# Performance work log

Measured on AMD Instinct MI355X. Metric: run time of the kernel, lower is better.

Reference implementation:

```python
import jax, jax.numpy as jnp
import numpy as np

B, T, IN, H = 128, 1024, 256, 512


def setup_inputs() -> dict:
    key = jax.random.key(0)
    ks = jax.random.split(key, 16)
    w = lambda k, shape: (jax.random.normal(k, shape, jnp.float32) * 0.02)
    inp = {"embed": jax.random.normal(ks[0], (B, T, IN), jnp.float32)}
    in_dims = [IN, H, H]
    for l in range(3):
        inp[f"w_ih{l+1}"] = w(ks[1 + 4 * l], (4 * H, in_dims[l]))
        inp[f"w_hh{l+1}"] = w(ks[2 + 4 * l], (4 * H, H))
        inp[f"b_ih{l+1}"] = w(ks[3 + 4 * l], (4 * H,))
        inp[f"b_hh{l+1}"] = w(ks[4 + 4 * l], (4 * H,))
    inp["fc_w"] = w(ks[13], (IN, H))
    inp["fc_b"] = w(ks[14], (IN,))
    return inp


def _lstm_cell(x, h, c, w_ih, w_hh, b):
    # PyTorch LSTMCell: gates ordered (i, f, g, o)
    gates = x @ w_ih.T + h @ w_hh.T + b  # [B, 4H]
    i, f, g, o = jnp.split(gates, 4, axis=-1)
    c_new = jax.nn.sigmoid(f) * c + jax.nn.sigmoid(i) * jnp.tanh(g)
    h_new = jax.nn.sigmoid(o) * jnp.tanh(c_new)
    return h_new, c_new


def reference(embed, w_ih1, w_hh1, b_ih1, b_hh1, w_ih2, w_hh2, b_ih2, b_hh2,
              w_ih3, w_hh3, b_ih3, b_hh3, fc_w, fc_b):
    Bn = embed.shape[0]
    hidden = w_hh1.shape[1]
    b1, b2, b3 = b_ih1 + b_hh1, b_ih2 + b_hh2, b_ih3 + b_hh3
    z = jnp.zeros((Bn, hidden), embed.dtype)

    def step(carry, x_t):
        h1, c1, h2, c2, h3, c3 = carry
        h1, c1 = _lstm_cell(x_t, h1, c1, w_ih1, w_hh1, b1)
        h2, c2 = _lstm_cell(h1, h2, c2, w_ih2, w_hh2, b2)
        h3, c3 = _lstm_cell(h2, h3, c3, w_ih3, w_hh3, b3)
        return (h1, c1, h2, c2, h3, c3), None

    # loop runs for i in range(seq_length - 1)
    xs = jnp.swapaxes(embed[:, : embed.shape[1] - 1, :], 0, 1)  # [T-1, B, IN]
    carry, _ = jax.lax.scan(step, (z, z, z, z, z, z), xs)
    h3 = carry[4]
    output = h3 @ fc_w.T + fc_b  # only the final timestep's fc output survives
    return (embed, output)
```

## Files before the change

kernel.cpp:

```cpp
#include <hip/hip_runtime.h>

#define Bn 128
#define Tn 1024
#define INn 256
#define Hn 512
#define NB 256

typedef short bf16x8 __attribute__((ext_vector_type(8)));
typedef float f32x4 __attribute__((ext_vector_type(4)));

#define WPK_OFF  0u
#define BIAS_OFF 23068672u
#define H_OFF    23093248u
#define H3F_OFF  24666112u
#define BAR_OFF  24928256u

#define L0B 0u
#define L1B 3145728u
#define L2B 7340032u

__device__ __forceinline__ float sigm(float x) { return 1.0f / (1.0f + __expf(-x)); }
__device__ __forceinline__ unsigned short bf_hi(float x) {
  unsigned u = __builtin_bit_cast(unsigned, x);
  return (unsigned short)(u >> 16);
}
__device__ __forceinline__ float bf_f(unsigned short h) {
  unsigned u = ((unsigned)h) << 16;
  return __builtin_bit_cast(float, u);
}

__global__ void pack_weights(const float* __restrict__ wih1, const float* __restrict__ whh1,
                             const float* __restrict__ wih2, const float* __restrict__ whh2,
                             const float* __restrict__ wih3, const float* __restrict__ whh3,
                             unsigned short* __restrict__ wpk) {
  int gid = blockIdx.x * 256 + threadIdx.x;
  int rem, NCH, kih; size_t base, slab; const float *wih, *whh;
  if (gid < 196608)      { rem = gid;          base = L0B; slab = 24576; NCH = 24; kih = 256; wih = wih1; whh = whh1; }
  else if (gid < 458752) { rem = gid - 196608; base = L1B; slab = 32768; NCH = 32; kih = 512; wih = wih2; whh = whh2; }
  else if (gid < 720896) { rem = gid - 458752; base = L2B; slab = 32768; NCH = 32; kih = 512; wih = wih3; whh = whh3; }
  else return;
  const int lane = rem & 63; rem >>= 6;
  const int kc = rem % NCH; rem /= NCH;
  const int G = rem;
  const int n = lane & 15;
  const int g = n >> 2, jl = n & 3;
  const int r = g * 512 + G * 4 + jl;
  const int k0 = kc * 32 + (lane >> 4) * 8;
  const float* src = (k0 < kih) ? (wih + (size_t)r * kih + k0)
                                : (whh + (size_t)r * 512 + (k0 - kih));
  const size_t dhi = base + (size_t)G * slab + (size_t)kc * 512 + lane * 8;
  const size_t dlo = dhi + (size_t)NCH * 512;
#pragma unroll
  for (int e = 0; e < 8; ++e) {
    float w = src[e];
    unsigned short h = bf_hi(w);
    wpk[dhi + e] = h;
    wpk[dlo + e] = bf_hi(w - bf_f(h));
  }
}

__global__ void pack_bias(const float* __restrict__ bi1, const float* __restrict__ bh1,
                          const float* __restrict__ bi2, const float* __restrict__ bh2,
                          const float* __restrict__ bi3, const float* __restrict__ bh3,
                          float* __restrict__ bias) {
  int gid = blockIdx.x * 256 + threadIdx.x;
  if (gid >= 6144) return;
  int l = gid >> 11, r = gid & 2047;
  const float* bi = (l == 0) ? bi1 : (l == 1) ? bi2 : bi3;
  const float* bh = (l == 0) ? bh1 : (l == 1) ? bh2 : bh3;
  bias[gid] = bi[r] + bh[r];
}

__device__ __forceinline__ void gridbar(unsigned* bar, unsigned idx, int shard) {
  __syncthreads();
  if (threadIdx.x == 0) {
    asm volatile("" ::: "memory");
    unsigned o = __hip_atomic_fetch_add(bar + shard * 32, 1u, __ATOMIC_RELAXED, __HIP_MEMORY_SCOPE_AGENT);
    if (o == idx * 32u - 1u) {
      unsigned r = __hip_atomic_fetch_add(bar + 256, 1u, __ATOMIC_RELAXED, __HIP_MEMORY_SCOPE_AGENT);
      if (r == idx * 8u - 1u)
        __hip_atomic_store(bar + 288, idx, __ATOMIC_RELAXED, __HIP_MEMORY_SCOPE_AGENT);
    }
    while (__hip_atomic_load(bar + 288, __ATOMIC_RELAXED, __HIP_MEMORY_SCOPE_AGENT) < idx)
      __builtin_amdgcn_s_sleep(1);
    asm volatile("" ::: "memory");
  }
  __syncthreads();
}

__global__ __launch_bounds__(1024) void lstm_persist(
    const float* __restrict__ embed,
    const unsigned short* __restrict__ wpk,
    const float* __restrict__ bias,
    float* __restrict__ hsys,
    float* __restrict__ h3f,
    unsigned* __restrict__ bar)
{
  const int bid = blockIdx.x;
  const int shard = bid & 7;
  const int jt = bid & 31;
  const int bt = bid >> 5;
  const int tid = (int)threadIdx.x;
  const int lane = tid & 63;
  const int w = tid >> 6;
  const int nsub = w & 3, kq = w >> 2;

  __shared__ short als[2][56][16][36];
  __shared__ float pre[2][4][16][65];
  __shared__ float sbias[3][64];

  if (tid < 192) {
    const int l = tid >> 6, c = tid & 63;
    const int n = c & 15, g = n >> 2;
    sbias[l][c] = bias[l * 2048 + g * 512 + jt * 16 + (c >> 4) * 4 + (n & 3)];
  }
  unsigned long long* hz = (unsigned long long*)hsys;
  for (int i = bid * 1024 + tid; i < 196608; i += NB * 1024)
    __hip_atomic_store(hz + i, 0ull, __ATOMIC_RELAXED, __HIP_MEMORY_SCOPE_SYSTEM);

  float c0 = 0.f, c1 = 0.f, c2 = 0.f;
  unsigned bidx = 1;
  gridbar(bar, bidx++, shard);

  const unsigned long long* hs_u = (const unsigned long long*)hsys;
  const int arow = lane & 15;
  const int kg8 = (lane >> 4) * 8;

  auto mfma_layer = [&](int NCH, int q4, size_t wbase, size_t slab, int lbase, int pl) {
    const int G = jt * 4 + nsub;
    const unsigned short* wb = wpk + wbase + (size_t)G * slab + (size_t)lane * 8;
    f32x4 accE = {0.f,0.f,0.f,0.f}, accO = {0.f,0.f,0.f,0.f};
#pragma unroll
    for (int i = 0; i < 8; ++i) {
      if (i >= q4) break;
      const int kc = kq * q4 + i;
      const int ch = lbase + kc;
      const bf16x8 aH = *reinterpret_cast<const bf16x8*>(&als[0][ch][arow][kg8]);
      const bf16x8 aL = *reinterpret_cast<const bf16x8*>(&als[1][ch][arow][kg8]);
      const bf16x8 bH = *reinterpret_cast<const bf16x8*>(wb + (size_t)kc * 512);
      const bf16x8 bL = *reinterpret_cast<const bf16x8*>(wb + (size_t)(NCH + kc) * 512);
      if (i & 1) {
        accO = __builtin_amdgcn_mfma_f32_16x16x32_bf16(aH, bH, accO, 0, 0, 0);
        accO = __builtin_amdgcn_mfma_f32_16x16x32_bf16(aL, bH, accO, 0, 0, 0);
        accO = __builtin_amdgcn_mfma_f32_16x16x32_bf16(aH, bL, accO, 0, 0, 0);
        accO = __builtin_amdgcn_mfma_f32_16x16x32_bf16(aL, bL, accO, 0, 0, 0);
      } else {
        accE = __builtin_amdgcn_mfma_f32_16x16x32_bf16(aH, bH, accE, 0, 0, 0);
        accE = __builtin_amdgcn_mfma_f32_16x16x32_bf16(aL, bH, accE, 0, 0, 0);
        accE = __builtin_amdgcn_mfma_f32_16x16x32_bf16(aH, bL, accE, 0, 0, 0);
        accE = __builtin_amdgcn_mfma_f32_16x16x32_bf16(aL, bL, accE, 0, 0, 0);
      }
    }
    const int prow = (lane >> 4) << 2;
    const int pc = lane & 15;
#pragma unroll
    for (int r = 0; r < 4; ++r)
      pre[pl][kq][prow + r][nsub * 16 + pc] = accE[r] + accO[r];
  };

  auto cell_layer = [&](int l, int pl, int wp, int t, float& c) {
    const int b = tid >> 4, jl = tid & 15;
    float gv[4];
#pragma unroll
    for (int gi = 0; gi < 4; ++gi) {
      const int cc = (jl >> 2) * 16 + gi * 4 + (jl & 3);
      gv[gi] = sbias[l][cc] + pre[pl][0][b][cc] + pre[pl][1][b][cc]
             + pre[pl][2][b][cc] + pre[pl][3][b][cc];
    }
    const float ig = sigm(gv[0]), fg = sigm(gv[1]), gg = tanhf(gv[2]), og = sigm(gv[3]);
    c = fg * c + ig * gg;
    const float hv = og * tanhf(c);
    __hip_atomic_store((unsigned*)hsys +
        ((size_t)(l * 2 + wp) * 65536 + (size_t)(bt * 16 + b) * 512 + jt * 16 + jl),
        __builtin_bit_cast(unsigned, hv), __ATOMIC_RELAXED, __HIP_MEMORY_SCOPE_SYSTEM);
    if (l == 2 && t == 1022)
      h3f[(size_t)(bt * 16 + b) * 512 + jt * 16 + jl] = hv;
  };

  for (int p = 0; p <= 1024; ++p) {
    const int rp = (p + 1) & 1, wp = p & 1;
    const bool a0 = (p <= 1022), a1 = (p >= 1) && (p <= 1023), a2 = (p >= 2);

    for (int u = tid; u < 3584; u += 1024) {
      float xs[8];
      int ch, row, ko;
      if (u < 512) {
        if (p > 1022) continue;
        row = u >> 5;
        const int k0 = (u & 31) << 3;
        const float* s = embed + ((size_t)(bt * 16 + row) * Tn + p) * INn + k0;
        const f32x4 x0 = __builtin_nontemporal_load(reinterpret_cast<const f32x4*>(s));
        const f32x4 x1 = __builtin_nontemporal_load(reinterpret_cast<const f32x4*>(s) + 1);
        xs[0]=x0.x; xs[1]=x0.y; xs[2]=x0.z; xs[3]=x0.w;
        xs[4]=x1.x; xs[5]=x1.y; xs[6]=x1.z; xs[7]=x1.w;
        ch = k0 >> 5; ko = k0 & 31;
      } else {
        const int v = u - 512;
        const int li = v >> 10;
        const int idx = v & 1023;
        row = idx >> 6;
        const int k0 = (idx & 63) << 3;
        const unsigned long long* sp = hs_u +
            ((size_t)(li * 2 + rp) * 32768 + (size_t)(bt * 16 + row) * 256 + (k0 >> 1));
#pragma unroll
        for (int q = 0; q < 4; ++q) {
          unsigned long long vv = __hip_atomic_load(sp + q, __ATOMIC_RELAXED, __HIP_MEMORY_SCOPE_SYSTEM);
          xs[2*q]   = __builtin_bit_cast(float, (unsigned)(vv & 0xffffffffu));
          xs[2*q+1] = __builtin_bit_cast(float, (unsigned)(vv >> 32));
        }
        ch = 8 + li * 16 + (k0 >> 5); ko = k0 & 31;
      }
      bf16x8 vh, vl;
#pragma unroll
      for (int e = 0; e < 8; ++e) {
        unsigned short h1 = bf_hi(xs[e]);
        vh[e] = (short)h1;
        vl[e] = (short)bf_hi(xs[e] - bf_f(h1));
      }
      *reinterpret_cast<bf16x8*>(&als[0][ch][row][ko]) = vh;
      *reinterpret_cast<bf16x8*>(&als[1][ch][row][ko]) = vl;
    }
    __syncthreads();

    if (a0) mfma_layer(24, 6, L0B, 24576, 0, 0);
    if (a1) mfma_layer(32, 8, L1B, 32768, 8, 1);
    __syncthreads();
    if (tid < 256) {
      if (a0) cell_layer(0, 0, wp, p, c0);
      if (a1) cell_layer(1, 1, wp, p - 1, c1);
    }
    __syncthreads();

    if (a2) mfma_layer(32, 8, L2B, 32768, 24, 0);
    __syncthreads();
    if (tid < 256 && a2) cell_layer(2, 0, wp, p - 2, c2);

    gridbar(bar, bidx++, shard);
  }
}

__global__ void fc_kernel(const float* __restrict__ h3f, const float* __restrict__ fcw,
                          const float* __restrict__ fcb, float* __restrict__ out) {
  const int gid = blockIdx.x * 256 + (int)threadIdx.x;
  if (gid >= Bn * INn) return;
  const int b = gid >> 8, o = gid & 255;
  const float* hr = h3f + (size_t)b * Hn;
  const float* wr = fcw + (size_t)o * Hn;
  float acc = fcb[o];
#pragma unroll 4
  for (int k = 0; k < Hn; k += 4) {
    const float4 hv = *reinterpret_cast<const float4*>(hr + k);
    const float4 wv = *reinterpret_cast<const float4*>(wr + k);
    acc = fmaf(hv.x, wv.x, acc); acc = fmaf(hv.y, wv.y, acc);
    acc = fmaf(hv.z, wv.z, acc); acc = fmaf(hv.w, wv.w, acc);
  }
  out[(size_t)Bn * Tn * INn + gid] = acc;
}

extern "C" void kernel_launch(void* const* d_in, const int* in_sizes, int n_in,
                              void* d_out, int out_size, void* d_ws, size_t ws_size,
                              hipStream_t stream) {
  const float* embed = (const float*)d_in[0];
  const float* wih1  = (const float*)d_in[1];
  const float* whh1  = (const float*)d_in[2];
  const float* bih1  = (const float*)d_in[3];
  const float* bhh1  = (const float*)d_in[4];
  const float* wih2  = (const float*)d_in[5];
  const float* whh2  = (const float*)d_in[6];
  const float* bih2  = (const float*)d_in[7];
  const float* bhh2  = (const float*)d_in[8];
  const float* wih3  = (const float*)d_in[9];
  const float* whh3  = (const float*)d_in[10];
  const float* bih3  = (const float*)d_in[11];
  const float* bhh3  = (const float*)d_in[12];
  const float* fcw   = (const float*)d_in[13];
  const float* fcb   = (const float*)d_in[14];
  float* outp = (float*)d_out;

  char* ws = (char*)d_ws;
  unsigned short* wpk = (unsigned short*)(ws + WPK_OFF);
  float* bias         = (float*)(ws + BIAS_OFF);
  float* hsys         = (float*)(ws + H_OFF);
  float* h3f          = (float*)(ws + H3F_OFF);
  unsigned* bar       = (unsigned*)(ws + BAR_OFF);

  hipMemcpyAsync(d_out, d_in[0], (size_t)Bn * Tn * INn * sizeof(float),
                 hipMemcpyDeviceToDevice, stream);
  hipMemsetAsync(bar, 0, 8192, stream);

  pack_weights<<<2816, 256, 0, stream>>>(wih1, whh1, wih2, whh2, wih3, whh3, wpk);
  pack_bias<<<24, 256, 0, stream>>>(bih1, bhh1, bih2, bhh2, bih3, bhh3, bias);

  void* args[] = { (void*)&embed, (void*)&wpk, (void*)&bias,
                   (void*)&hsys, (void*)&h3f, (void*)&bar };
  dim3 grid(NB), block(1024);
  hipLaunchCooperativeKernel((const void*)lstm_persist, grid, block, args, 0, stream);

  fc_kernel<<<128, 256, 0, stream>>>(h3f, fcw, fcb, outp);
}
```

Baseline: 19.68 ms.

## Split per-step grid barrier into two post/wait barriers to overlap phases

Replaces the single grid-wide barrier at the end of each timestep with two split-phase barriers. Barrier A is posted after the layer-0/1 cell updates, and barrier B after the layer-2 update. Each block waits only right before it reads the hidden states it depends on. The embed load for the next step is issued before any wait, and the layer-2 MFMA runs after posting A, so barrier latency overlaps useful work. This adds more barrier counters and a subtler dependency ordering on the double-buffered hidden state, which risks races if the buffers are reused too early.

Measured after the change: 20.30 ms. 3.1% more time.

```diff
diff --git a/kernel.cpp b/kernel.cpp
--- a/kernel.cpp
+++ b/kernel.cpp
@@ -71,7 +71,7 @@
   bias[gid] = bi[r] + bh[r];
 }
 
-__device__ __forceinline__ void gridbar(unsigned* bar, unsigned idx, int shard) {
+__device__ __forceinline__ void barpost(unsigned* bar, unsigned idx, int shard) {
   __syncthreads();
   if (threadIdx.x == 0) {
     asm volatile("" ::: "memory");
@@ -81,11 +81,19 @@
       if (r == idx * 8u - 1u)
         __hip_atomic_store(bar + 288, idx, __ATOMIC_RELAXED, __HIP_MEMORY_SCOPE_AGENT);
     }
+  }
+}
+__device__ __forceinline__ void barwait(unsigned* bar, unsigned idx) {
+  if (threadIdx.x == 0) {
     while (__hip_atomic_load(bar + 288, __ATOMIC_RELAXED, __HIP_MEMORY_SCOPE_AGENT) < idx)
       __builtin_amdgcn_s_sleep(1);
     asm volatile("" ::: "memory");
   }
   __syncthreads();
+}
+__device__ __forceinline__ void gridbar(unsigned* bar, unsigned idx, int shard) {
+  barpost(bar, idx, shard);
+  barwait(bar, idx);
 }
 
 __global__ __launch_bounds__(1024) void lstm_persist(
@@ -105,9 +113,13 @@
   const int w = tid >> 6;
   const int nsub = w & 3, kq = w >> 2;
 
-  __shared__ short als[2][56][16][36];
+  __shared__ short als[2][56][578];
   __shared__ float pre[2][4][16][65];
   __shared__ float sbias[3][64];
+
+  unsigned* barA = bar;
+  unsigned* barB = bar + 512;
+  unsigned* barI = bar + 1024;
 
   if (tid < 192) {
     const int l = tid >> 6, c = tid & 63;
@@ -119,8 +131,7 @@
     __hip_atomic_store(hz + i, 0ull, __ATOMIC_RELAXED, __HIP_MEMORY_SCOPE_SYSTEM);
 
   float c0 = 0.f, c1 = 0.f, c2 = 0.f;
-  unsigned bidx = 1;
-  gridbar(bar, bidx++, shard);
+  gridbar(barI, 1, shard);
 
   const unsigned long long* hs_u = (const unsigned long long*)hsys;
   const int arow = lane & 15;
@@ -135,8 +146,8 @@
       if (i >= q4) break;
       const int kc = kq * q4 + i;
       const int ch = lbase + kc;
-      const bf16x8 aH = *reinterpret_cast<const bf16x8*>(&als[0][ch][arow][kg8]);
-      const bf16x8 aL = *reinterpret_cast<const bf16x8*>(&als[1][ch][arow][kg8]);
+      const bf16x8 aH = *reinterpret_cast<const bf16x8*>(&als[0][ch][arow * 36 + kg8]);
+      const bf16x8 aL = *reinterpret_cast<const bf16x8*>(&als[1][ch][arow * 36 + kg8]);
       const bf16x8 bH = *reinterpret_cast<const bf16x8*>(wb + (size_t)kc * 512);
       const bf16x8 bL = *reinterpret_cast<const bf16x8*>(wb + (size_t)(NCH + kc) * 512);
       if (i & 1) {
@@ -177,48 +188,64 @@
       h3f[(size_t)(bt * 16 + b) * 512 + jt * 16 + jl] = hv;
   };
 
+  auto stage_write = [&](const float* xs, int ch, int row, int ko) {
+    bf16x8 vh, vl;
+#pragma unroll
+    for (int e = 0; e < 8; ++e) {
+      unsigned short h1 = bf_hi(xs[e]);
+      vh[e] = (short)h1;
+      vl[e] = (short)bf_hi(xs[e] - bf_f(h1));
+    }
+    *reinterpret_cast<bf16x8*>(&als[0][ch][row * 36 + ko]) = vh;
+    *reinterpret_cast<bf16x8*>(&als[1][ch][row * 36 + ko]) = vl;
+  };
+
   for (int p = 0; p <= 1024; ++p) {
     const int rp = (p + 1) & 1, wp = p & 1;
     const bool a0 = (p <= 1022), a1 = (p >= 1) && (p <= 1023), a2 = (p >= 2);
 
-    for (int u = tid; u < 3584; u += 1024) {
+    if (p <= 1022 && tid < 512) {
+      const int row = tid >> 5;
+      const int k0 = (tid & 31) << 3;
+      const float* s = embed + ((size_t)(bt * 16 + row) * Tn + p) * INn + k0;
+      const f32x4 x0 = __builtin_nontemporal_load(reinterpret_cast<const f32x4*>(s));
+      const f32x4 x1 = __builtin_nontemporal_load(reinterpret_cast<const f32x4*>(s) + 1);
+      float xs[8] = {x0.x, x0.y, x0.z, x0.w, x1.x, x1.y, x1.z, x1.w};
+      stage_write(xs, k0 >> 5, row, k0 & 31);
+    }
+
+    barwait(barA, (unsigned)p);
+    for (int u = tid; u < 2048; u += 1024) {
+      const int li = u >> 10;
+      const int idx2 = u & 1023;
+      const int row = idx2 >> 6;
+      const int k0 = (idx2 & 63) << 3;
+      const unsigned long long* sp = hs_u +
+          ((size_t)(li * 2 + rp) * 32768 + (size_t)(bt * 16 + row) * 256 + (k0 >> 1));
       float xs[8];
-      int ch, row, ko;
-      if (u < 512) {
-        if (p > 1022) continue;
-        row = u >> 5;
-        const int k0 = (u & 31) << 3;
-        const float* s = embed + ((size_t)(bt * 16 + row) * Tn + p) * INn + k0;
-        const f32x4 x0 = __builtin_nontemporal_load(reinterpret_cast<const f32x4*>(s));
-        const f32x4 x1 = __builtin_nontemporal_load(reinterpret_cast<const f32x4*>(s) + 1);
-        xs[0]=x0.x; xs[1]=x0.y; xs[2]=x0.z; xs[3]=x0.w;
-        xs[4]=x1.x; xs[5]=x1.y; xs[6]=x1.z; xs[7]=x1.w;
-        ch = k0 >> 5; ko = k0 & 31;
-      } else {
-        const int v = u - 512;
-        const int li = v >> 10;
-        const int idx = v & 1023;
-        row = idx >> 6;
-        const int k0 = (idx & 63) << 3;
-        const unsigned long long* sp = hs_u +
-            ((size_t)(li * 2 + rp) * 32768 + (size_t)(bt * 16 + row) * 256 + (k0 >> 1));
-#pragma unroll
-        for (int q = 0; q < 4; ++q) {
-          unsigned long long vv = __hip_atomic_load(sp + q, __ATOMIC_RELAXED, __HIP_MEMORY_SCOPE_SYSTEM);
-          xs[2*q]   = __builtin_bit_cast(float, (unsigned)(vv & 0xffffffffu));
-          xs[2*q+1] = __builtin_bit_cast(float, (unsigned)(vv >> 32));
-        }
-        ch = 8 + li * 16 + (k0 >> 5); ko = k0 & 31;
+#pragma unroll
+      for (int q = 0; q < 4; ++q) {
+        unsigned long long vv = __hip_atomic_load(sp + q, __ATOMIC_RELAXED, __HIP_MEMORY_SCOPE_SYSTEM);
+        xs[2*q]   = __builtin_bit_cast(float, (unsigned)(vv & 0xffffffffu));
+        xs[2*q+1] = __builtin_bit_cast(float, (unsigned)(vv >> 32));
       }
-      bf16x8 vh, vl;
-#pragma unroll
-      for (int e = 0; e < 8; ++e) {
-        unsigned short h1 = bf_hi(xs[e]);
-        vh[e] = (short)h1;
-        vl[e] = (short)bf_hi(xs[e] - bf_f(h1));
+      stage_write(xs, 8 + li * 16 + (k0 >> 5), row, k0 & 31);
+    }
+
+    barwait(barB, (unsigned)p);
+    {
+      const int row = tid >> 6;
+      const int k0 = (tid & 63) << 3;
+      const unsigned long long* sp = hs_u +
+          ((size_t)(2 * 2 + rp) * 32768 + (size_t)(bt * 16 + row) * 256 + (k0 >> 1));
+      float xs[8];
+#pragma unroll
+      for (int q = 0; q < 4; ++q) {
+        unsigned long long vv = __hip_atomic_load(sp + q, __ATOMIC_RELAXED, __HIP_MEMORY_SCOPE_SYSTEM);
+        xs[2*q]   = __builtin_bit_cast(float, (unsigned)(vv & 0xffffffffu));
+        xs[2*q+1] = __builtin_bit_cast(float, (unsigned)(vv >> 32));
       }
-      *reinterpret_cast<bf16x8*>(&als[0][ch][row][ko]) = vh;
-      *reinterpret_cast<bf16x8*>(&als[1][ch][row][ko]) = vl;
+      stage_write(xs, 40 + (k0 >> 5), row, k0 & 31);
     }
     __syncthreads();
 
@@ -229,13 +256,12 @@
       if (a0) cell_layer(0, 0, wp, p, c0);
       if (a1) cell_layer(1, 1, wp, p - 1, c1);
     }
-    __syncthreads();
+    barpost(barA, (unsigned)p + 1u, shard);
 
     if (a2) mfma_layer(32, 8, L2B, 32768, 24, 0);
     __syncthreads();
     if (tid < 256 && a2) cell_layer(2, 0, wp, p - 2, c2);
-
-    gridbar(bar, bidx++, shard);
+    barpost(barB, (unsigned)p + 1u, shard);
   }
 }
 
```
